# Kernel tuning notes

Measured on AMD Instinct MI355X. Metric: run time of the kernel, lower is better.

The kernel has to match this reference:

```python
import jax, jax.numpy as jnp
import numpy as np

N_HEAD = 16

def apply_rope(t, cos, sin):
    # t: [B, H, T, hd]; cos/sin: [T, hd//2] -> broadcast [1,1,T,hd//2]
    hd = t.shape[-1]
    t1, t2 = t[..., : hd // 2], t[..., hd // 2 :]
    c = cos[None, None, :, :]
    s = sin[None, None, :, :]
    return jnp.concatenate([t1 * c - t2 * s, t1 * s + t2 * c], axis=-1)

def setup_inputs() -> dict:
    key = jax.random.key(0)
    k1, k2, k3, k4, k5 = jax.random.split(key, 5)
    B, T, C = 2, 2048, 2048
    hd = C // N_HEAD
    x = jax.random.normal(k1, (B, T, C), dtype=jnp.float32)
    cos = jax.random.uniform(k2, (T, hd // 2), dtype=jnp.float32)
    sin = jax.random.uniform(k3, (T, hd // 2), dtype=jnp.float32)
    W_attn = jax.random.normal(k4, (C, 3 * C), dtype=jnp.float32) * (1.0 / np.sqrt(C))
    W_proj = jax.random.normal(k5, (C, C), dtype=jnp.float32) * (1.0 / np.sqrt(C))
    return {"x": x, "cos": cos, "sin": sin, "W_attn": W_attn, "W_proj": W_proj}

def reference(x, cos, sin, W_attn, W_proj):
    B, T, C = x.shape
    hd = C // N_HEAD
    qkv = jnp.einsum("btc,cd->btd", x, W_attn)  # [B,T,3C]
    q, k, v = jnp.split(qkv, 3, axis=-1)
    # [B,T,C] -> [B,H,T,hd]
    def to_heads(t):
        return t.reshape(B, T, N_HEAD, hd).transpose(0, 2, 1, 3)
    q, k, v = to_heads(q), to_heads(k), to_heads(v)
    q = apply_rope(q, cos[:T], sin[:T])
    k = apply_rope(k, cos[:T], sin[:T])
    scale = 1.0 / np.sqrt(hd).astype(np.float32)
    scores = jnp.einsum("bhqd,bhkd->bhqk", q, k) * scale
    causal = jnp.tril(jnp.ones((T, T), dtype=bool))
    scores = jnp.where(causal[None, None], scores, jnp.finfo(scores.dtype).min)
    attn = jax.nn.softmax(scores, axis=-1)
    y = jnp.einsum("bhqk,bhkd->bhqd", attn, v)  # [B,H,T,hd]
    y = y.transpose(0, 2, 1, 3).reshape(B, T, C)
    return jnp.einsum("btc,cd->btd", y, W_proj)
```

## Files before the change

### kernel.cpp

```cpp
#include <hip/hip_runtime.h>
#include <stdint.h>

typedef unsigned short u16;
typedef __bf16 v8bf __attribute__((ext_vector_type(8)));
typedef float f32x4 __attribute__((ext_vector_type(4)));

#define MFMA16(a, b, c) __builtin_amdgcn_mfma_f32_16x16x32_bf16((a), (b), (c), 0, 0, 0)

typedef const __attribute__((address_space(1))) uint32_t* gp32;
typedef __attribute__((address_space(3))) uint32_t* lp32;
#define ASYNC16(g, l) __builtin_amdgcn_global_load_lds((gp32)(const void*)(g), (lp32)(void*)(l), 16, 0, 0)

__device__ __forceinline__ u16 f2bf(float f) {
  union { float f; uint32_t u; } v; v.f = f;
  uint32_t r = v.u + 0x7fffu + ((v.u >> 16) & 1u);
  return (u16)(r >> 16);
}
__device__ __forceinline__ float bf2f(u16 h) {
  union { uint32_t u; float f; } v; v.u = ((uint32_t)h) << 16;
  return v.f;
}

__device__ __forceinline__ int swK(int r, int lc) {
  return r * 128 + (((lc ^ (r & 7)) & 15) << 3);
}
__device__ __forceinline__ int swV(int r, int lc) {
  return r * 64 + (((lc ^ (r & 7)) & 7) << 3);
}

__device__ __forceinline__ void transpose_tile(const float* __restrict__ in,
                                               u16* __restrict__ out, int R, int Cc,
                                               int bx, int by, int tid,
                                               u16 (*tile)[34]) {
  int c0 = bx * 32, r0 = by * 32;
  int tx = tid & 31, ty = tid >> 5;
#pragma unroll
  for (int i = 0; i < 32; i += 8)
    tile[ty + i][tx] = f2bf(in[(size_t)(r0 + ty + i) * Cc + c0 + tx]);
  __syncthreads();
#pragma unroll
  for (int i = 0; i < 32; i += 8)
    out[(size_t)(c0 + ty + i) * R + r0 + tx] = tile[tx][ty + i];
}

__global__ __launch_bounds__(256) void prep_kernel(const float* __restrict__ x,
                                                   u16* __restrict__ xb,
                                                   const float* __restrict__ Wa,
                                                   u16* __restrict__ WaT,
                                                   const float* __restrict__ Wp,
                                                   u16* __restrict__ WpT) {
  __shared__ u16 tile[32][34];
  int bid = blockIdx.x;
  int tid = threadIdx.x;
  if (bid < 4096) {
    int i = (bid * 256 + tid) * 8;
    float4 a = *(const float4*)(x + i);
    float4 b = *(const float4*)(x + i + 4);
    uint4 o;
    o.x = (uint32_t)f2bf(a.x) | ((uint32_t)f2bf(a.y) << 16);
    o.y = (uint32_t)f2bf(a.z) | ((uint32_t)f2bf(a.w) << 16);
    o.z = (uint32_t)f2bf(b.x) | ((uint32_t)f2bf(b.y) << 16);
    o.w = (uint32_t)f2bf(b.z) | ((uint32_t)f2bf(b.w) << 16);
    *(uint4*)(xb + i) = o;
  } else if (bid < 4096 + 12288) {
    int t = bid - 4096;
    transpose_tile(Wa, WaT, 2048, 6144, t % 192, t / 192, tid, tile);
  } else {
    int t = bid - 16384;
    transpose_tile(Wp, WpT, 2048, 2048, t & 63, t >> 6, tid, tile);
  }
}

template <typename OutT>
__global__ __launch_bounds__(256) void gemm_bt(const u16* __restrict__ A,
                                               const u16* __restrict__ Bt,
                                               OutT* __restrict__ C, int M, int N, int K) {
  __shared__ u16 As[128 * 64];
  __shared__ u16 Bs[128 * 64];
  int tid = threadIdx.x;
  int wave = tid >> 6, lane = tid & 63, quad = lane >> 4, l16 = lane & 15;
  int wr = wave >> 1, wc = wave & 1;
  int m0 = blockIdx.y * 128, n0 = blockIdx.x * 128;
  f32x4 acc[4][4] = {};
  int lrow = lane >> 3, lk = lane & 7;
  int lc = lk ^ lrow;
  const u16* Ab = A + (size_t)m0 * K;
  const u16* Bb = Bt + (size_t)n0 * K;

  for (int k0 = 0; k0 < K; k0 += 64) {
#pragma unroll
    for (int j = 0; j < 4; ++j) {
      int rbase = wave * 32 + j * 8;
      int row = rbase + lrow;
      ASYNC16(Ab + (size_t)row * K + k0 + lc * 8, &As[rbase * 64]);
      ASYNC16(Bb + (size_t)row * K + k0 + lc * 8, &Bs[rbase * 64]);
    }
    __syncthreads();
#pragma unroll
    for (int ks = 0; ks < 2; ++ks) {
      v8bf af[4], bfr[4];
#pragma unroll
      for (int t = 0; t < 4; ++t) {
        af[t]  = *(const v8bf*)&As[swV(wr * 64 + t * 16 + l16, ks * 4 + quad)];
        bfr[t] = *(const v8bf*)&Bs[swV(wc * 64 + t * 16 + l16, ks * 4 + quad)];
      }
#pragma unroll
      for (int mt = 0; mt < 4; ++mt)
#pragma unroll
        for (int nt = 0; nt < 4; ++nt)
          acc[mt][nt] = MFMA16(af[mt], bfr[nt], acc[mt][nt]);
    }
    __syncthreads();
  }
#pragma unroll
  for (int mt = 0; mt < 4; ++mt)
#pragma unroll
    for (int nt = 0; nt < 4; ++nt) {
      int row = m0 + wr * 64 + mt * 16 + quad * 4;
      int col = n0 + wc * 64 + nt * 16 + l16;
#pragma unroll
      for (int r = 0; r < 4; ++r) {
        float v = acc[mt][nt][r];
        if constexpr (sizeof(OutT) == 2)
          C[(size_t)(row + r) * N + col] = (OutT)f2bf(v);
        else
          C[(size_t)(row + r) * N + col] = v;
      }
    }
}

__global__ __launch_bounds__(256) void gemm_qkv_rope(const u16* __restrict__ A,
                                                     const u16* __restrict__ Bt,
                                                     const float* __restrict__ cosp,
                                                     const float* __restrict__ sinp,
                                                     u16* __restrict__ qh,
                                                     u16* __restrict__ kh,
                                                     u16* __restrict__ vt) {
  const int K = 2048, T = 2048;
  __shared__ u16 smem[128 * 130];
  u16* As = smem;
  u16* Bs = smem + 128 * 64;
  int tid = threadIdx.x;
  int wave = tid >> 6, lane = tid & 63, quad = lane >> 4, l16 = lane & 15;
  int wr = wave >> 1, wc = wave & 1;
  int m0 = blockIdx.y * 128, n0 = blockIdx.x * 128;
  f32x4 acc[4][4] = {};
  int lrow = lane >> 3, lk = lane & 7;
  int lc = lk ^ lrow;
  const u16* Ab = A + (size_t)m0 * K;
  const u16* Bb = Bt + (size_t)n0 * K;

  for (int k0 = 0; k0 < K; k0 += 64) {
#pragma unroll
    for (int j = 0; j < 4; ++j) {
      int rbase = wave * 32 + j * 8;
      int row = rbase + lrow;
      ASYNC16(Ab + (size_t)row * K + k0 + lc * 8, &As[rbase * 64]);
      ASYNC16(Bb + (size_t)row * K + k0 + lc * 8, &Bs[rbase * 64]);
    }
    __syncthreads();
#pragma unroll
    for (int ks = 0; ks < 2; ++ks) {
      v8bf af[4], bfr[4];
#pragma unroll
      for (int t = 0; t < 4; ++t) {
        af[t]  = *(const v8bf*)&As[swV(wr * 64 + t * 16 + l16, ks * 4 + quad)];
        bfr[t] = *(const v8bf*)&Bs[swV(wc * 64 + t * 16 + l16, ks * 4 + quad)];
      }
#pragma unroll
      for (int mt = 0; mt < 4; ++mt)
#pragma unroll
        for (int nt = 0; nt < 4; ++nt)
          acc[mt][nt] = MFMA16(af[mt], bfr[nt], acc[mt][nt]);
    }
    __syncthreads();
  }

#pragma unroll
  for (int mt = 0; mt < 4; ++mt)
#pragma unroll
    for (int nt = 0; nt < 4; ++nt) {
      int rloc = wr * 64 + mt * 16 + quad * 4;
      int cloc = wc * 64 + nt * 16 + l16;
#pragma unroll
      for (int r = 0; r < 4; ++r)
        smem[(rloc + r) * 130 + cloc] = f2bf(acc[mt][nt][r]);
    }
  __syncthreads();

  int sec = (int)blockIdx.x >> 4;
  int h   = (int)blockIdx.x & 15;
  int b   = m0 >> 11;
  int t0  = m0 & 2047;
  int bh  = b * 16 + h;

  if (sec < 2) {
    u16* dst = sec ? kh : qh;
    const float QSCL = 0.08838834764831845f * 1.4426950408889634f;
    float scl = sec ? 1.0f : QSCL;
    int j = tid & 63, tl0 = tid >> 6;
#pragma unroll 4
    for (int i = 0; i < 32; ++i) {
      int tl = i * 4 + tl0;
      int t  = t0 + tl;
      float c = cosp[t * 64 + j], s = sinp[t * 64 + j];
      float x1 = bf2f(smem[tl * 130 + j]);
      float x2 = bf2f(smem[tl * 130 + 64 + j]);
      size_t o = ((size_t)bh * T + t) * 128;
      dst[o + j]      = f2bf((x1 * c - x2 * s) * scl);
      dst[o + 64 + j] = f2bf((x1 * s + x2 * c) * scl);
    }
  } else {
    int l = tid & 63, w = tid >> 6;
#pragma unroll 4
    for (int i = 0; i < 32; ++i) {
      int d = i * 4 + w;
      size_t o = ((size_t)bh * 128 + d) * T + t0;
      vt[o + l]      = smem[l * 130 + d];
      vt[o + 64 + l] = smem[(64 + l) * 130 + d];
    }
  }
}

__global__ __launch_bounds__(512) void flash_attn(const u16* __restrict__ qh,
                                                  const u16* __restrict__ kh,
                                                  const u16* __restrict__ vt,
                                                  u16* __restrict__ yh) {
  __shared__ u16 Ks[2][64 * 128];
  __shared__ u16 Vs[2][128 * 64];
  __shared__ u16 Pb[128 * 64];
  const int T = 2048, HD = 128;
  int tid = threadIdx.x;
  int wave = tid >> 6, lane = tid & 63, quad = lane >> 4, l16 = lane & 15;
  int bh = blockIdx.y, b = bh >> 4, h = bh & 15;
  const u16* qb = qh + (size_t)bh * T * HD;
  const u16* kb = kh + (size_t)bh * T * HD;
  const u16* vb = vt + (size_t)bh * HD * T;
  int krow_off = lane >> 4, kchunk = lane & 15;
  int vrow_off = lane >> 3, vchunk = lane & 7;

  for (int tp = 0; tp < 2; ++tp) {
    int qt = tp ? 15 - (int)blockIdx.x : (int)blockIdx.x;
    int q0 = qt * 128;
    int n_it = 2 * qt + 2;

    v8bf qf[4];
#pragma unroll
    for (int ks = 0; ks < 4; ++ks)
      qf[ks] = *(const v8bf*)&qb[(size_t)(q0 + wave * 16 + l16) * HD + ks * 32 + quad * 8];

    f32x4 acc[8] = {};
    float rs_p[4] = {};
    uint4 vreg[2];

#pragma unroll
    for (int j = 0; j < 2; ++j) {
      int rbase = wave * 8 + j * 4;
      int r = rbase + krow_off;
      int lc = kchunk ^ (r & 7);
      ASYNC16(kb + (size_t)r * HD + lc * 8, &Ks[0][rbase * 128]);
    }
#pragma unroll
    for (int j = 0; j < 2; ++j) {
      int row = wave * 16 + j * 8 + vrow_off;
      int lc = vchunk ^ (row & 7);
      vreg[j] = *(const uint4*)&vb[(size_t)row * T + lc * 8];
    }
#pragma unroll
    for (int j = 0; j < 2; ++j) {
      int row = wave * 16 + j * 8 + vrow_off;
      *(uint4*)&Vs[0][row * 64 + vchunk * 8] = vreg[j];
    }
    __syncthreads();

    for (int it = 0; it < n_it; ++it) {
      int c = it & 1;

      if (it + 1 < n_it) {
        int kv0n = (it + 1) * 64;
#pragma unroll
        for (int j = 0; j < 2; ++j) {
          int rbase = wave * 8 + j * 4;
          int r = rbase + krow_off;
          int lc = kchunk ^ (r & 7);
          ASYNC16(kb + (size_t)(kv0n + r) * HD + lc * 8, &Ks[1 - c][rbase * 128]);
        }
#pragma unroll
        for (int j = 0; j < 2; ++j) {
          int row = wave * 16 + j * 8 + vrow_off;
          int lc = vchunk ^ (row & 7);
          vreg[j] = *(const uint4*)&vb[(size_t)row * T + kv0n + lc * 8];
        }
      }

      f32x4 s[4] = {};
#pragma unroll
      for (int ks = 0; ks < 4; ++ks)
#pragma unroll
        for (int nt = 0; nt < 4; ++nt) {
          v8bf kf = *(const v8bf*)&Ks[c][swK(nt * 16 + l16, ks * 4 + quad)];
          s[nt] = MFMA16(qf[ks], kf, s[nt]);
        }

      if (it >= 2 * qt) {
        int kv0 = it * 64;
#pragma unroll
        for (int r = 0; r < 4; ++r) {
          int row = q0 + wave * 16 + quad * 4 + r;
#pragma unroll
          for (int nt = 0; nt < 4; ++nt)
            if (kv0 + nt * 16 + l16 > row) s[nt][r] = -1e30f;
        }
      }

#pragma unroll
      for (int nt = 0; nt < 4; ++nt)
#pragma unroll
        for (int r = 0; r < 4; ++r) {
          float p = __builtin_exp2f(s[nt][r]);
          rs_p[r] += p;
          int row = wave * 16 + quad * 4 + r;
          int col = nt * 16 + l16;
          Pb[row * 64 + ((((col >> 3) ^ (row & 7)) & 7) << 3) + (col & 7)] = f2bf(p);
        }

#pragma unroll
      for (int ks = 0; ks < 2; ++ks) {
        v8bf pa = *(const v8bf*)&Pb[swV(wave * 16 + l16, ks * 4 + quad)];
#pragma unroll
        for (int dt = 0; dt < 8; ++dt) {
          v8bf vf = *(const v8bf*)&Vs[c][swV(dt * 16 + l16, ks * 4 + quad)];
          acc[dt] = MFMA16(pa, vf, acc[dt]);
        }
      }

      if (it + 1 < n_it) {
#pragma unroll
        for (int j = 0; j < 2; ++j) {
          int row = wave * 16 + j * 8 + vrow_off;
          *(uint4*)&Vs[1 - c][row * 64 + vchunk * 8] = vreg[j];
        }
      }

      __syncthreads();
    }

#pragma unroll
    for (int r = 0; r < 4; ++r) {
      float rsv = rs_p[r];
      rsv += __shfl_xor(rsv, 1);
      rsv += __shfl_xor(rsv, 2);
      rsv += __shfl_xor(rsv, 4);
      rsv += __shfl_xor(rsv, 8);
      float inv = 1.f / rsv;
      int t = q0 + wave * 16 + quad * 4 + r;
#pragma unroll
      for (int dt = 0; dt < 8; ++dt)
        yh[(size_t)(b * T + t) * 2048 + h * 128 + dt * 16 + l16] = f2bf(acc[dt][r] * inv);
    }
  }
}

extern "C" void kernel_launch(void* const* d_in, const int* in_sizes, int n_in,
                              void* d_out, int out_size, void* d_ws, size_t ws_size,
                              hipStream_t stream) {
  const float* x    = (const float*)d_in[0];
  const float* cosp = (const float*)d_in[1];
  const float* sinp = (const float*)d_in[2];
  const float* Wa   = (const float*)d_in[3];
  const float* Wp   = (const float*)d_in[4];
  float* out = (float*)d_out;

  char* ws = (char*)d_ws;
  u16* xb  = (u16*)(ws);
  u16* WaT = (u16*)(ws + (size_t)(16 << 20));
  u16* WpT = (u16*)(ws + (size_t)(40 << 20));
  u16* qh  = (u16*)(ws + (size_t)(48 << 20));
  u16* kh  = (u16*)(ws + (size_t)(64 << 20));
  u16* vt  = (u16*)(ws + (size_t)(80 << 20));
  u16* yh  = (u16*)(ws + (size_t)(96 << 20));

  prep_kernel<<<20480, 256, 0, stream>>>(x, xb, Wa, WaT, Wp, WpT);
  gemm_qkv_rope<<<dim3(48, 32), 256, 0, stream>>>(xb, WaT, cosp, sinp, qh, kh, vt);
  flash_attn<<<dim3(8, 32), 512, 0, stream>>>(qh, kh, vt, yh);
  gemm_bt<float><<<dim3(16, 32), 256, 0, stream>>>(yh, WpT, out, 4096, 2048, 2048);
}
```

Before: 396.0 us.

## Read K/V fragments directly from global and launch one query tile per block

The attention kernel drops the double-buffered LDS staging of K and V tiles, along with the async copies and per-iteration barriers. Each wave now loads its MFMA operand fragments straight from global memory, relying on the caches. The grid doubles so each block handles a single 128-row query tile, and the tile order is reversed for half the heads to spread the causal work. This removes barrier and LDS-copy overhead and frees LDS for more resident blocks. The cost is eight times more redundant K/V fetches per block and no prefetching to hide global-load latency.

```diff
diff --git a/kernel.cpp b/kernel.cpp
--- a/kernel.cpp
+++ b/kernel.cpp
@@ -21,9 +21,6 @@
   return v.f;
 }
 
-__device__ __forceinline__ int swK(int r, int lc) {
-  return r * 128 + (((lc ^ (r & 7)) & 15) << 3);
-}
 __device__ __forceinline__ int swV(int r, int lc) {
   return r * 64 + (((lc ^ (r & 7)) & 7) << 3);
 }
@@ -226,8 +223,6 @@
                                                   const u16* __restrict__ kh,
                                                   const u16* __restrict__ vt,
                                                   u16* __restrict__ yh) {
-  __shared__ u16 Ks[2][64 * 128];
-  __shared__ u16 Vs[2][128 * 64];
   __shared__ u16 Pb[128 * 64];
   const int T = 2048, HD = 128;
   int tid = threadIdx.x;
@@ -236,128 +231,75 @@
   const u16* qb = qh + (size_t)bh * T * HD;
   const u16* kb = kh + (size_t)bh * T * HD;
   const u16* vb = vt + (size_t)bh * HD * T;
-  int krow_off = lane >> 4, kchunk = lane & 15;
-  int vrow_off = lane >> 3, vchunk = lane & 7;
-
-  for (int tp = 0; tp < 2; ++tp) {
-    int qt = tp ? 15 - (int)blockIdx.x : (int)blockIdx.x;
-    int q0 = qt * 128;
-    int n_it = 2 * qt + 2;
-
-    v8bf qf[4];
+
+  int qt = (bh < 16) ? 15 - (int)blockIdx.x : (int)blockIdx.x;
+  int q0 = qt * 128;
+  int n_it = 2 * qt + 2;
+
+  v8bf qf[4];
+#pragma unroll
+  for (int ks = 0; ks < 4; ++ks)
+    qf[ks] = *(const v8bf*)&qb[(size_t)(q0 + wave * 16 + l16) * HD + ks * 32 + quad * 8];
+
+  f32x4 acc[8] = {};
+  float rs_p[4] = {};
+
+  for (int it = 0; it < n_it; ++it) {
+    int kv0 = it * 64;
+
+    f32x4 s[4] = {};
 #pragma unroll
     for (int ks = 0; ks < 4; ++ks)
-      qf[ks] = *(const v8bf*)&qb[(size_t)(q0 + wave * 16 + l16) * HD + ks * 32 + quad * 8];
-
-    f32x4 acc[8] = {};
-    float rs_p[4] = {};
-    uint4 vreg[2];
-
-#pragma unroll
-    for (int j = 0; j < 2; ++j) {
-      int rbase = wave * 8 + j * 4;
-      int r = rbase + krow_off;
-      int lc = kchunk ^ (r & 7);
-      ASYNC16(kb + (size_t)r * HD + lc * 8, &Ks[0][rbase * 128]);
-    }
-#pragma unroll
-    for (int j = 0; j < 2; ++j) {
-      int row = wave * 16 + j * 8 + vrow_off;
-      int lc = vchunk ^ (row & 7);
-      vreg[j] = *(const uint4*)&vb[(size_t)row * T + lc * 8];
-    }
-#pragma unroll
-    for (int j = 0; j < 2; ++j) {
-      int row = wave * 16 + j * 8 + vrow_off;
-      *(uint4*)&Vs[0][row * 64 + vchunk * 8] = vreg[j];
-    }
-    __syncthreads();
-
-    for (int it = 0; it < n_it; ++it) {
-      int c = it & 1;
-
-      if (it + 1 < n_it) {
-        int kv0n = (it + 1) * 64;
-#pragma unroll
-        for (int j = 0; j < 2; ++j) {
-          int rbase = wave * 8 + j * 4;
-          int r = rbase + krow_off;
-          int lc = kchunk ^ (r & 7);
-          ASYNC16(kb + (size_t)(kv0n + r) * HD + lc * 8, &Ks[1 - c][rbase * 128]);
-        }
-#pragma unroll
-        for (int j = 0; j < 2; ++j) {
-          int row = wave * 16 + j * 8 + vrow_off;
-          int lc = vchunk ^ (row & 7);
-          vreg[j] = *(const uint4*)&vb[(size_t)row * T + kv0n + lc * 8];
-        }
-      }
-
-      f32x4 s[4] = {};
-#pragma unroll
-      for (int ks = 0; ks < 4; ++ks)
-#pragma unroll
-        for (int nt = 0; nt < 4; ++nt) {
-          v8bf kf = *(const v8bf*)&Ks[c][swK(nt * 16 + l16, ks * 4 + quad)];
-          s[nt] = MFMA16(qf[ks], kf, s[nt]);
-        }
-
-      if (it >= 2 * qt) {
-        int kv0 = it * 64;
-#pragma unroll
-        for (int r = 0; r < 4; ++r) {
-          int row = q0 + wave * 16 + quad * 4 + r;
-#pragma unroll
-          for (int nt = 0; nt < 4; ++nt)
-            if (kv0 + nt * 16 + l16 > row) s[nt][r] = -1e30f;
-        }
-      }
-
-#pragma unroll
-      for (int nt = 0; nt < 4; ++nt)
-#pragma unroll
-        for (int r = 0; r < 4; ++r) {
-          float p = __builtin_exp2f(s[nt][r]);
-          rs_p[r] += p;
-          int row = wave * 16 + quad * 4 + r;
-          int col = nt * 16 + l16;
-          Pb[row * 64 + ((((col >> 3) ^ (row & 7)) & 7) << 3) + (col & 7)] = f2bf(p);
-        }
-
-#pragma unroll
-      for (int ks = 0; ks < 2; ++ks) {
-        v8bf pa = *(const v8bf*)&Pb[swV(wave * 16 + l16, ks * 4 + quad)];
-#pragma unroll
-        for (int dt = 0; dt < 8; ++dt) {
-          v8bf vf = *(const v8bf*)&Vs[c][swV(dt * 16 + l16, ks * 4 + quad)];
-          acc[dt] = MFMA16(pa, vf, acc[dt]);
-        }
-      }
-
-      if (it + 1 < n_it) {
-#pragma unroll
-        for (int j = 0; j < 2; ++j) {
-          int row = wave * 16 + j * 8 + vrow_off;
-          *(uint4*)&Vs[1 - c][row * 64 + vchunk * 8] = vreg[j];
-        }
-      }
-
-      __syncthreads();
-    }
-
-#pragma unroll
-    for (int r = 0; r < 4; ++r) {
-      float rsv = rs_p[r];
-      rsv += __shfl_xor(rsv, 1);
-      rsv += __shfl_xor(rsv, 2);
-      rsv += __shfl_xor(rsv, 4);
-      rsv += __shfl_xor(rsv, 8);
-      float inv = 1.f / rsv;
-      int t = q0 + wave * 16 + quad * 4 + r;
-#pragma unroll
-      for (int dt = 0; dt < 8; ++dt)
-        yh[(size_t)(b * T + t) * 2048 + h * 128 + dt * 16 + l16] = f2bf(acc[dt][r] * inv);
-    }
+#pragma unroll
+      for (int nt = 0; nt < 4; ++nt) {
+        v8bf kf = *(const v8bf*)&kb[(size_t)(kv0 + nt * 16 + l16) * HD + ks * 32 + quad * 8];
+        s[nt] = MFMA16(qf[ks], kf, s[nt]);
+      }
+
+    if (it >= 2 * qt) {
+#pragma unroll
+      for (int r = 0; r < 4; ++r) {
+        int row = q0 + wave * 16 + quad * 4 + r;
+#pragma unroll
+        for (int nt = 0; nt < 4; ++nt)
+          if (kv0 + nt * 16 + l16 > row) s[nt][r] = -1e30f;
+      }
+    }
+
+#pragma unroll
+    for (int nt = 0; nt < 4; ++nt)
+#pragma unroll
+      for (int r = 0; r < 4; ++r) {
+        float p = __builtin_exp2f(s[nt][r]);
+        rs_p[r] += p;
+        int row = wave * 16 + quad * 4 + r;
+        int col = nt * 16 + l16;
+        Pb[row * 64 + ((((col >> 3) ^ (row & 7)) & 7) << 3) + (col & 7)] = f2bf(p);
+      }
+
+#pragma unroll
+    for (int ks = 0; ks < 2; ++ks) {
+      v8bf pa = *(const v8bf*)&Pb[swV(wave * 16 + l16, ks * 4 + quad)];
+#pragma unroll
+      for (int dt = 0; dt < 8; ++dt) {
+        v8bf vf = *(const v8bf*)&vb[(size_t)(dt * 16 + l16) * T + kv0 + ks * 32 + quad * 8];
+        acc[dt] = MFMA16(pa, vf, acc[dt]);
+      }
+    }
+  }
+
+#pragma unroll
+  for (int r = 0; r < 4; ++r) {
+    float rsv = rs_p[r];
+    rsv += __shfl_xor(rsv, 1);
+    rsv += __shfl_xor(rsv, 2);
+    rsv += __shfl_xor(rsv, 4);
+    rsv += __shfl_xor(rsv, 8);
+    float inv = 1.f / rsv;
+    int t = q0 + wave * 16 + quad * 4 + r;
+#pragma unroll
+    for (int dt = 0; dt < 8; ++dt)
+      yh[(size_t)(b * T + t) * 2048 + h * 128 + dt * 16 + l16] = f2bf(acc[dt][r] * inv);
   }
 }
 
@@ -382,6 +324,6 @@
 
   prep_kernel<<<20480, 256, 0, stream>>>(x, xb, Wa, WaT, Wp, WpT);
   gemm_qkv_rope<<<dim3(48, 32), 256, 0, stream>>>(xb, WaT, cosp, sinp, qh, kh, vt);
-  flash_attn<<<dim3(8, 32), 512, 0, stream>>>(qh, kh, vt, yh);
+  flash_attn<<<dim3(16, 32), 512, 0, stream>>>(qh, kh, vt, yh);
   gemm_bt<float><<<dim3(16, 32), 256, 0, stream>>>(yh, WpT, out, 4096, 2048, 2048);
 }
```

Measured after the change: 551.2 us. 39.2% more time.
